# Optimization experiments

Hardware: AMD Instinct MI355X
Metric: run time of the kernel (lower is better)

## Reference

```python
import jax, jax.numpy as jnp
import numpy as np

C = 96        # d_model
DI = 192      # d_inner = 2*C
N = 16        # d_state
R = 6         # dt_rank = ceil(C/16)
K = 4         # scan directions
B_, H_, W_ = 2, 48, 48


def setup_inputs():
    key = jax.random.key(0)
    ks = jax.random.split(key, 12)
    def rn(k, shape, s=0.02):
        return jax.random.normal(k, shape, jnp.float32) * s
    # S4D-real A init and realistic dt bias (inverse softplus of dt in [1e-3, 1e-1])
    A = jnp.tile(jnp.arange(1, N + 1, dtype=jnp.float32), (K, DI, 1))
    dt = jax.random.uniform(ks[0], (K, DI), jnp.float32, 1e-3, 1e-1)
    inv_softplus_dt = dt + jnp.log(-jnp.expm1(-dt))
    return {
        "x": jax.random.normal(ks[1], (B_, C, H_, W_), jnp.float32),
        "ln1_w": jnp.ones((C,), jnp.float32), "ln1_b": jnp.zeros((C,), jnp.float32),
        "in_proj_w": rn(ks[2], (2 * DI, C)),
        "conv_w": rn(ks[3], (DI, 1, 3, 3), 0.1), "conv_b": jnp.zeros((DI,), jnp.float32),
        "x_proj_w": rn(ks[4], (K, R + 2 * N, DI)),
        "dt_proj_w": rn(ks[5], (K, DI, R), 0.1), "dt_proj_b": inv_softplus_dt,
        "A_log": jnp.log(A), "Ds": jnp.ones((K, DI), jnp.float32),
        "out_norm_w": jnp.ones((DI,), jnp.float32), "out_norm_b": jnp.zeros((DI,), jnp.float32),
        "out_proj_w": rn(ks[6], (C, DI)),
        "ln2_w": jnp.ones((C,), jnp.float32), "ln2_b": jnp.zeros((C,), jnp.float32),
        "fc1_w": rn(ks[7], (C, C)), "fc1_b": jnp.zeros((C,), jnp.float32),
        "fc2_w": rn(ks[8], (C, C)), "fc2_b": jnp.zeros((C,), jnp.float32),
        "proj_w": rn(ks[9], (1, C)), "proj_b": jnp.zeros((1,), jnp.float32),
    }


def _layernorm(x, w, b, eps=1e-5):
    mu = x.mean(-1, keepdims=True)
    var = x.var(-1, keepdims=True)
    return (x - mu) * jax.lax.rsqrt(var + eps) * w + b


def _selective_scan(u, delta, A, Bm, Cm, D):
    # u, delta: (B,K,D,L); A: (K,D,N); Bm, Cm: (B,K,N,L); D: (K,D)
    dA = jnp.exp(jnp.einsum('bkdl,kdn->lbkdn', delta, A))
    dBu = jnp.einsum('bkdl,bknl->lbkdn', delta * u, Bm)
    Ct = jnp.moveaxis(Cm, -1, 0)  # (L,B,K,N)
    h0 = jnp.zeros(dA.shape[1:], u.dtype)
    def step(h, inp):
        dA_t, dBu_t, C_t = inp
        h = dA_t * h + dBu_t
        y = jnp.einsum('bkdn,bkn->bkd', h, C_t)
        return h, y
    _, ys = jax.lax.scan(step, h0, (dA, dBu, Ct))
    y = jnp.moveaxis(ys, 0, -1)  # (B,K,D,L)
    return y + u * D[None, :, :, None]


def _ss2d(x, in_proj_w, conv_w, conv_b, x_proj_w, dt_proj_w, dt_proj_b,
          A_log, Ds, out_norm_w, out_norm_b, out_proj_w):
    Bsz, H, W, _ = x.shape
    L = H * W
    xz = x @ in_proj_w.T                      # (B,H,W,2*DI)
    xh, z = jnp.split(xz, 2, axis=-1)
    xc = xh.transpose(0, 3, 1, 2)             # (B,DI,H,W)
    xc = jax.lax.conv_general_dilated(
        xc, conv_w, (1, 1), ((1, 1), (1, 1)),
        feature_group_count=DI,
        dimension_numbers=('NCHW', 'OIHW', 'NCHW')) + conv_b[None, :, None, None]
    xc = jax.nn.silu(xc)
    # cross-scan: 4 directions (row-major, col-major, and their reverses)
    xf = xc.reshape(Bsz, DI, L)
    xt = xc.transpose(0, 1, 3, 2).reshape(Bsz, DI, L)
    xs2 = jnp.stack([xf, xt], axis=1)
    xs = jnp.concatenate([xs2, jnp.flip(xs2, axis=-1)], axis=1)   # (B,4,DI,L)
    x_dbl = jnp.einsum('bkdl,kcd->bkcl', xs, x_proj_w)
    dts, Bm, Cm = jnp.split(x_dbl, [R, R + N], axis=2)
    delta = jnp.einsum('bkrl,kdr->bkdl', dts, dt_proj_w) + dt_proj_b[None, :, :, None]
    delta = jax.nn.softplus(delta)
    A = -jnp.exp(A_log)
    out_y = _selective_scan(xs, delta, A, Bm, Cm, Ds)             # (B,4,DI,L)
    # cross-merge: undo flips/transposes and sum
    inv_y = jnp.flip(out_y[:, 2:4], axis=-1)
    wh_y = out_y[:, 1].reshape(Bsz, DI, W, H).transpose(0, 1, 3, 2).reshape(Bsz, DI, L)
    invwh_y = inv_y[:, 1].reshape(Bsz, DI, W, H).transpose(0, 1, 3, 2).reshape(Bsz, DI, L)
    y = out_y[:, 0] + inv_y[:, 0] + wh_y + invwh_y                # (B,DI,L)
    y = _layernorm(y.transpose(0, 2, 1), out_norm_w, out_norm_b).reshape(Bsz, H, W, DI)
    y = y * jax.nn.silu(z)
    return y @ out_proj_w.T


def reference(x, ln1_w, ln1_b, in_proj_w, conv_w, conv_b, x_proj_w, dt_proj_w,
              dt_proj_b, A_log, Ds, out_norm_w, out_norm_b, out_proj_w,
              ln2_w, ln2_b, fc1_w, fc1_b, fc2_w, fc2_b, proj_w, proj_b):
    xh = x.transpose(0, 2, 3, 1)   # (B,H,W,C)
    # VSSBlock (pre-norm): x = x + SS2D(LN(x)); x = x + MLP(LN(x))
    h1 = _layernorm(xh, ln1_w, ln1_b)
    xh = xh + _ss2d(h1, in_proj_w, conv_w, conv_b, x_proj_w, dt_proj_w,
                    dt_proj_b, A_log, Ds, out_norm_w, out_norm_b, out_proj_w)
    h2 = _layernorm(xh, ln2_w, ln2_b)
    xh = xh + (jax.nn.gelu(h2 @ fc1_w.T + fc1_b, approximate=False) @ fc2_w.T + fc2_b)
    # 1x1 conv projector + sigmoid
    y = xh @ proj_w.T + proj_b     # (B,H,W,1)
    return jax.nn.sigmoid(y).transpose(0, 3, 1, 2)
```

## Files before the change

kernel.cpp:

```cpp
#include <hip/hip_runtime.h>
#include <cstdint>

static constexpr int LSZ = 2304;
static constexpr int CBS = 96;
static constexpr int DIN = 192;
static constexpr int NST = 16;
static constexpr int HHT = 48;
static constexpr int WWD = 48;
static constexpr int CHN = 16;
static constexpr int CHL = 144;

static constexpr size_t OFF_XCONV = 0;
static constexpr size_t OFF_SILUZ = 884736;
static constexpr size_t OFF_XC    = 1769472;
static constexpr size_t OFF_XCT   = 2654208;
static constexpr size_t OFF_BCT   = 3686400;
static constexpr size_t OFF_DELTA = 4276224;
static constexpr size_t OFF_YK    = 7815168;
static constexpr size_t OFF_WT    = 11796480;

__device__ __forceinline__ float f4get(const float4& v, int i) {
    return i == 0 ? v.x : i == 1 ? v.y : i == 2 ? v.z : v.w;
}

__device__ __forceinline__ float rotadd16(float v) {
    int m;
    m = __builtin_amdgcn_update_dpp(0, __float_as_int(v), 0x128, 0xf, 0xf, false); v += __int_as_float(m);
    m = __builtin_amdgcn_update_dpp(0, __float_as_int(v), 0x124, 0xf, 0xf, false); v += __int_as_float(m);
    m = __builtin_amdgcn_update_dpp(0, __float_as_int(v), 0x122, 0xf, 0xf, false); v += __int_as_float(m);
    m = __builtin_amdgcn_update_dpp(0, __float_as_int(v), 0x121, 0xf, 0xf, false); v += __int_as_float(m);
    return v;
}

__global__ __launch_bounds__(256) void kPrep(const float* __restrict__ Wp,
    const float* __restrict__ Wo, const float* __restrict__ W1,
    const float* __restrict__ W2, float* __restrict__ wt) {
    int e = blockIdx.x * 256 + threadIdx.x;
    if (e < 36864) {
        int c = e / 384, t = e % 384;
        wt[e] = Wp[t * 96 + c];
    } else if (e < 55296) {
        int e2 = e - 36864; int dd = e2 / 96, cc = e2 % 96;
        wt[e] = Wo[cc * 192 + dd];
    } else if (e < 64512) {
        int e2 = e - 55296; int jj = e2 / 96, ii = e2 % 96;
        wt[e] = W1[ii * 96 + jj];
    } else if (e < 73728) {
        int e2 = e - 64512; int jj = e2 / 96, ii = e2 % 96;
        wt[e] = W2[ii * 96 + jj];
    }
}

__global__ __launch_bounds__(384) void kA(const float* __restrict__ x,
    const float* __restrict__ ln1w, const float* __restrict__ ln1b,
    const float* __restrict__ Wt, float* __restrict__ xconv, float* __restrict__ siluz) {
    int blk = blockIdx.x; int b = blk / 144; int s0 = (blk % 144) * 16;
    int tid = threadIdx.x;
    __shared__ float xln[96][20];
    __shared__ float mu16[16], ir16[16];
#pragma unroll
    for (int it = 0; it < 4; ++it) {
        int e = it * 384 + tid; int c = e >> 4, si = e & 15;
        xln[c][si] = x[((size_t)b * CBS + c) * LSZ + s0 + si];
    }
    __syncthreads();
    if (tid < 16) {
        float s1 = 0.f, s2 = 0.f;
#pragma unroll 8
        for (int c = 0; c < 96; ++c) { float v = xln[c][tid]; s1 += v; s2 += v * v; }
        float mu = s1 * (1.f / 96.f);
        mu16[tid] = mu; ir16[tid] = rsqrtf(s2 * (1.f / 96.f) - mu * mu + 1e-5f);
    }
    __syncthreads();
#pragma unroll
    for (int it = 0; it < 4; ++it) {
        int e = it * 384 + tid; int c = e >> 4, si = e & 15;
        xln[c][si] = (xln[c][si] - mu16[si]) * ir16[si] * ln1w[c] + ln1b[c];
    }
    __syncthreads();
    float acc[16];
#pragma unroll
    for (int i = 0; i < 16; ++i) acc[i] = 0.f;
    for (int c = 0; c < 96; ++c) {
        float wv = Wt[c * 384 + tid];
#pragma unroll
        for (int i = 0; i < 16; ++i) acc[i] = fmaf(wv, xln[c][i], acc[i]);
    }
    if (tid < DIN) {
        size_t base = ((size_t)b * DIN + tid) * LSZ + s0;
#pragma unroll
        for (int q = 0; q < 4; ++q) {
            float4 v = make_float4(acc[4 * q], acc[4 * q + 1], acc[4 * q + 2], acc[4 * q + 3]);
            *(float4*)(xconv + base + 4 * q) = v;
        }
    } else {
        int t = tid - DIN;
#pragma unroll
        for (int si = 0; si < 16; ++si) {
            float z = acc[si];
            siluz[((size_t)b * LSZ + s0 + si) * DIN + t] = z / (1.f + __expf(-z));
        }
    }
}

__global__ __launch_bounds__(256) void kB(const float* __restrict__ xconv,
    const float* __restrict__ cw, const float* __restrict__ cb,
    float* __restrict__ xc, float* __restrict__ xcT) {
    int bd = blockIdx.x;
    int d = bd % DIN;
    int tid = threadIdx.x;
    __shared__ float inp[2304];
    __shared__ float outp[48 * 49];
    const float* src = xconv + (size_t)bd * LSZ;
#pragma unroll
    for (int i = 0; i < 9; ++i) inp[i * 256 + tid] = src[i * 256 + tid];
    float w0 = cw[d * 9 + 0], w1 = cw[d * 9 + 1], w2 = cw[d * 9 + 2];
    float w3 = cw[d * 9 + 3], w4 = cw[d * 9 + 4], w5 = cw[d * 9 + 5];
    float w6 = cw[d * 9 + 6], w7 = cw[d * 9 + 7], w8 = cw[d * 9 + 8];
    float bias = cb[d];
    __syncthreads();
#pragma unroll
    for (int i = 0; i < 9; ++i) {
        int s = i * 256 + tid; int h = s / 48, w = s % 48;
        float acc = bias;
        bool hn = h > 0, hp = h < 47, wn = w > 0, wp = w < 47;
        if (hn) {
            if (wn) acc = fmaf(inp[s - 49], w0, acc);
            acc = fmaf(inp[s - 48], w1, acc);
            if (wp) acc = fmaf(inp[s - 47], w2, acc);
        }
        if (wn) acc = fmaf(inp[s - 1], w3, acc);
        acc = fmaf(inp[s], w4, acc);
        if (wp) acc = fmaf(inp[s + 1], w5, acc);
        if (hp) {
            if (wn) acc = fmaf(inp[s + 47], w6, acc);
            acc = fmaf(inp[s + 48], w7, acc);
            if (wp) acc = fmaf(inp[s + 49], w8, acc);
        }
        float r = acc / (1.f + __expf(-acc));
        xc[(size_t)bd * LSZ + s] = r;
        outp[h * 49 + w] = r;
    }
    __syncthreads();
#pragma unroll
    for (int i = 0; i < 9; ++i) {
        int p = i * 256 + tid;
        int w = p / 48, h = p % 48;
        xcT[(size_t)bd * LSZ + p] = outp[h * 49 + w];
    }
}

__global__ __launch_bounds__(256) void kC(const float* __restrict__ xc,
    const float* __restrict__ xcT, const float* __restrict__ xpw,
    const float* __restrict__ dtw, const float* __restrict__ dtb,
    float* __restrict__ BCt, float* __restrict__ delta) {
    int blk = blockIdx.x; int lt = blk % 36; int k = (blk / 36) & 3; int b = blk / 144;
    int l0 = lt * 64;
    int bk = b * 4 + k;
    __shared__ float xs[DIN][64];
    __shared__ float stage[64][33];
    __shared__ float dtrL[6][64];
    __shared__ float wsh[DIN * 6];
    __shared__ float bshL[DIN];
    const float* src = ((k & 1) ? xcT : xc) + (size_t)b * DIN * LSZ;
    bool fwd = (k < 2);
    int tid = threadIdx.x;
    for (int e = tid; e < 1152; e += 256) wsh[e] = dtw[k * 1152 + e];
    if (tid < DIN) bshL[tid] = dtb[k * DIN + tid];
#pragma unroll
    for (int i = 0; i < 48; ++i) {
        int e = i * 256 + tid; int d = e >> 6, ll = e & 63;
        int l = l0 + ll; int sl = fwd ? l : (LSZ - 1 - l);
        xs[d][ll] = src[(size_t)d * LSZ + sl];
    }
    __syncthreads();
    int c0 = tid >> 6, ll = tid & 63;
    float acc[10];
#pragma unroll
    for (int j = 0; j < 10; ++j) acc[j] = 0.f;
    for (int d0 = 0; d0 < DIN; d0 += 16) {
        float xv[16];
#pragma unroll
        for (int i = 0; i < 16; ++i) xv[i] = xs[d0 + i][ll];
#pragma unroll
        for (int j = 0; j < 10; ++j) {
            int c = j * 4 + c0;
            if (c < 38) {
                const float4* wr = (const float4*)(xpw + ((size_t)(k * 38 + c)) * DIN + d0);
                float4 q0 = wr[0], q1 = wr[1], q2 = wr[2], q3 = wr[3];
                acc[j] += xv[0] * q0.x + xv[1] * q0.y + xv[2] * q0.z + xv[3] * q0.w
                        + xv[4] * q1.x + xv[5] * q1.y + xv[6] * q1.z + xv[7] * q1.w
                        + xv[8] * q2.x + xv[9] * q2.y + xv[10] * q2.z + xv[11] * q2.w
                        + xv[12] * q3.x + xv[13] * q3.y + xv[14] * q3.z + xv[15] * q3.w;
            }
        }
    }
#pragma unroll
    for (int j = 0; j < 10; ++j) {
        int c = j * 4 + c0;
        if (c < 6) {
            dtrL[c][ll] = acc[j];
        } else if (c < 38) {
            int n2 = (c < 22) ? (c - 6) : (16 + c - 22);
            stage[ll][n2] = acc[j];
        }
    }
    __syncthreads();
    float* dst = BCt + ((size_t)bk * LSZ + l0) * 32;
#pragma unroll
    for (int it = 0; it < 8; ++it) {
        int e = it * 256 + tid;
        int l = e >> 5, n2 = e & 31;
        dst[e] = stage[l][n2];
    }
    int dsub = tid >> 6;
    float dr[6];
#pragma unroll
    for (int r = 0; r < 6; ++r) dr[r] = dtrL[r][ll];
    for (int j = 0; j < 48; ++j) {
        int d = j * 4 + dsub;
        float a2 = bshL[d];
#pragma unroll
        for (int r = 0; r < 6; ++r) a2 = fmaf(dr[r], wsh[d * 6 + r], a2);
        float sp = (a2 > 20.f) ? a2 : log1pf(__expf(a2));
        delta[((size_t)bk * DIN + d) * LSZ + l0 + ll] = sp;
    }
}

__global__ __launch_bounds__(256, 4) void kD(const float* __restrict__ delta,
    const float* __restrict__ xc, const float* __restrict__ xcT,
    const float* __restrict__ BCt, const float* __restrict__ A_log, float* __restrict__ yk) {
    int g = blockIdx.x;
    int tid = threadIdx.x;
    int n = tid & 15; int c = tid >> 4;
    int d = g % DIN; int bk = g / DIN; int k = bk & 3; int b = bk >> 2;
    __shared__ float hfinL[256];
    __shared__ float sumdL[16];
    __shared__ float hinL[256];

    float An2 = -__expf(A_log[((size_t)(k * DIN + d)) * NST + n]) * 1.44269504f;
    const float* ub = ((k & 1) ? xcT : xc) + ((size_t)(b * DIN + d)) * LSZ;
    bool fwd = (k < 2);
    int l0 = c * CHL;
    const float* dp = delta + (size_t)g * LSZ + l0;
    const float* up = fwd ? (ub + l0) : (ub + (LSZ - 4) - l0);
    const float* bc = BCt + ((size_t)bk * LSZ + l0) * 32 + n;

    float h = 0.f, sd = 0.f;
    for (int j0 = 0; j0 < CHL; j0 += 4) {
        float4 dv = *(const float4*)(dp + j0);
        float4 uv;
        if (fwd) uv = *(const float4*)(up + j0);
        else { float4 tv = *(const float4*)(up - j0); uv = make_float4(tv.w, tv.z, tv.y, tv.x); }
#pragma unroll
        for (int jj = 0; jj < 4; ++jj) {
            float bn = bc[(j0 + jj) * 32];
            float dl = f4get(dv, jj);
            float da = __builtin_amdgcn_exp2f(dl * An2);
            h = fmaf(da, h, dl * f4get(uv, jj) * bn);
            sd += dl;
        }
    }
    hfinL[tid] = h;
    if (n == 0) sumdL[c] = sd;
    __syncthreads();

    if (tid < 16) {
        float hh = 0.f;
#pragma unroll
        for (int cc = 0; cc < 16; ++cc) {
            hinL[cc * 16 + tid] = hh;
            hh = fmaf(__builtin_amdgcn_exp2f(An2 * sumdL[cc]), hh, hfinL[cc * 16 + tid]);
        }
    }
    __syncthreads();

    h = hinL[tid];
    float* yo = yk + (size_t)g * LSZ + l0 + n;
    for (int m = 0; m < 9; ++m) {
        float ykeep = 0.f;
        for (int q = 0; q < 4; ++q) {
            int j0 = m * 16 + q * 4;
            float4 dv = *(const float4*)(dp + j0);
            float4 uv;
            if (fwd) uv = *(const float4*)(up + j0);
            else { float4 tv = *(const float4*)(up - j0); uv = make_float4(tv.w, tv.z, tv.y, tv.x); }
#pragma unroll
            for (int jj = 0; jj < 4; ++jj) {
                float bn = bc[(j0 + jj) * 32];
                float cn = bc[(j0 + jj) * 32 + 16];
                float dl = f4get(dv, jj);
                float da = __builtin_amdgcn_exp2f(dl * An2);
                h = fmaf(da, h, dl * f4get(uv, jj) * bn);
                float p = rotadd16(h * cn);
                ykeep = (n == q * 4 + jj) ? p : ykeep;
            }
        }
        yo[m * 16] = ykeep;
    }
}

__global__ __launch_bounds__(256) void kM(const float* __restrict__ yk,
    const float* __restrict__ xc, const float* __restrict__ Dsp, float* __restrict__ ym) {
    int blk = blockIdx.x;
    int b = blk / DIN; int d = blk % DIN;
    int tid = threadIdx.x;
    __shared__ float buf[4][48 * 49];
    float Dsum = Dsp[d] + Dsp[DIN + d] + Dsp[2 * DIN + d] + Dsp[3 * DIN + d];
#pragma unroll
    for (int kk = 0; kk < 4; ++kk) {
        const float* src = yk + ((size_t)((b * 4 + kk) * DIN + d)) * LSZ;
#pragma unroll
        for (int i = 0; i < 9; ++i) {
            int s = i * 256 + tid;
            buf[kk][s + s / 48] = src[s];
        }
    }
    __syncthreads();
    const float* xrow = xc + ((size_t)(b * DIN + d)) * LSZ;
    float* dst = ym + ((size_t)blk) * LSZ;
#pragma unroll
    for (int i = 0; i < 9; ++i) {
        int s = i * 256 + tid; int hh = s / 48, ww = s % 48;
        float v0 = buf[0][hh * 49 + ww];
        float v2 = buf[2][(47 - hh) * 49 + (47 - ww)];
        float v1 = buf[1][ww * 49 + hh];
        float v3 = buf[3][(47 - ww) * 49 + (47 - hh)];
        dst[s] = v0 + v2 + v1 + v3 + Dsum * xrow[s];
    }
}

__global__ __launch_bounds__(192) void kEF(const float* __restrict__ ym,
    const float* __restrict__ siluz, const float* __restrict__ x,
    const float* __restrict__ onw, const float* __restrict__ onb,
    const float* __restrict__ WoT,
    const float* __restrict__ l2w, const float* __restrict__ l2b,
    const float* __restrict__ W1T, const float* __restrict__ b1,
    const float* __restrict__ W2T, const float* __restrict__ b2,
    const float* __restrict__ pw, const float* __restrict__ pb, float* __restrict__ out) {
    int blk = blockIdx.x; int b = blk / 144; int s0 = (blk % 144) * 16;
    int tid = threadIdx.x;
    __shared__ float yl[DIN][17];
    __shared__ float xo[96][17];
    __shared__ float aa[96][17];
    __shared__ float mu16[16], ir16[16];
#pragma unroll
    for (int it = 0; it < 16; ++it) {
        int e = it * 192 + tid; int d = e >> 4, si = e & 15;
        yl[d][si] = ym[((size_t)(b * DIN + d)) * LSZ + s0 + si];
    }
    __syncthreads();
    if (tid < 16) {
        float s1 = 0.f, s2 = 0.f;
        for (int c = 0; c < DIN; ++c) { float v = yl[c][tid]; s1 += v; s2 += v * v; }
        float mu = s1 * (1.f / 192.f);
        mu16[tid] = mu; ir16[tid] = rsqrtf(s2 * (1.f / 192.f) - mu * mu + 1e-5f);
    }
    __syncthreads();
#pragma unroll
    for (int si = 0; si < 16; ++si) {
        float v = yl[tid][si];
        v = (v - mu16[si]) * ir16[si] * onw[tid] + onb[tid];
        yl[tid][si] = v * siluz[((size_t)b * LSZ + s0 + si) * DIN + tid];
    }
    __syncthreads();
    int tp = tid % 96, half = tid / 96;
    {
        float acc[8];
#pragma unroll
        for (int i = 0; i < 8; ++i) acc[i] = 0.f;
        for (int d2 = 0; d2 < DIN; ++d2) {
            float wv = WoT[d2 * 96 + tp];
#pragma unroll
            for (int i = 0; i < 8; ++i) acc[i] = fmaf(wv, yl[d2][half * 8 + i], acc[i]);
        }
#pragma unroll
        for (int i = 0; i < 8; ++i) {
            int si = half * 8 + i;
            xo[tp][si] = x[((size_t)b * CBS + tp) * LSZ + s0 + si] + acc[i];
        }
    }
    __syncthreads();
    if (tid < 16) {
        float s1 = 0.f, s2 = 0.f;
        for (int c = 0; c < 96; ++c) { float v = xo[c][tid]; s1 += v; s2 += v * v; }
        float mu = s1 * (1.f / 96.f);
        mu16[tid] = mu; ir16[tid] = rsqrtf(s2 * (1.f / 96.f) - mu * mu + 1e-5f);
    }
    __syncthreads();
#pragma unroll
    for (int it = 0; it < 8; ++it) {
        int e = it * 192 + tid; int si = e / 96, cc = e % 96;
        aa[cc][si] = (xo[cc][si] - mu16[si]) * ir16[si] * l2w[cc] + l2b[cc];
    }
    __syncthreads();
    float acc[8];
#pragma unroll
    for (int i = 0; i < 8; ++i) acc[i] = 0.f;
    for (int j = 0; j < 96; ++j) {
        float wv = W1T[j * 96 + tp];
#pragma unroll
        for (int i = 0; i < 8; ++i) acc[i] = fmaf(wv, aa[j][half * 8 + i], acc[i]);
    }
    __syncthreads();
#pragma unroll
    for (int i = 0; i < 8; ++i) {
        float tv = acc[i] + b1[tp];
        aa[tp][half * 8 + i] = 0.5f * tv * (1.f + erff(tv * 0.70710678118654752f));
    }
    __syncthreads();
    float acc2[8];
#pragma unroll
    for (int i = 0; i < 8; ++i) acc2[i] = 0.f;
    for (int j = 0; j < 96; ++j) {
        float wv = W2T[j * 96 + tp];
#pragma unroll
        for (int i = 0; i < 8; ++i) acc2[i] = fmaf(wv, aa[j][half * 8 + i], acc2[i]);
    }
    __syncthreads();
#pragma unroll
    for (int i = 0; i < 8; ++i) {
        float xf = xo[tp][half * 8 + i] + acc2[i] + b2[tp];
        aa[tp][half * 8 + i] = xf * pw[tp];
    }
    __syncthreads();
    if (tid < 16) {
        float ssum = 0.f;
        for (int c = 0; c < 96; ++c) ssum += aa[c][tid];
        out[(size_t)b * LSZ + s0 + tid] = 1.f / (1.f + __expf(-(ssum + pb[0])));
    }
}

extern "C" void kernel_launch(void* const* d_in, const int* in_sizes, int n_in,
                              void* d_out, int out_size, void* d_ws, size_t ws_size,
                              hipStream_t stream) {
    const float* x    = (const float*)d_in[0];
    const float* ln1w = (const float*)d_in[1];
    const float* ln1b = (const float*)d_in[2];
    const float* Wp   = (const float*)d_in[3];
    const float* cw   = (const float*)d_in[4];
    const float* cb   = (const float*)d_in[5];
    const float* xpw  = (const float*)d_in[6];
    const float* dtw  = (const float*)d_in[7];
    const float* dtb  = (const float*)d_in[8];
    const float* Alog = (const float*)d_in[9];
    const float* Dsp  = (const float*)d_in[10];
    const float* onw  = (const float*)d_in[11];
    const float* onb  = (const float*)d_in[12];
    const float* Wo   = (const float*)d_in[13];
    const float* l2w  = (const float*)d_in[14];
    const float* l2b  = (const float*)d_in[15];
    const float* W1   = (const float*)d_in[16];
    const float* b1   = (const float*)d_in[17];
    const float* W2   = (const float*)d_in[18];
    const float* b2   = (const float*)d_in[19];
    const float* pw   = (const float*)d_in[20];
    const float* pb   = (const float*)d_in[21];

    float* ws    = (float*)d_ws;
    float* xconv = ws + OFF_XCONV;
    float* ym    = ws + OFF_XCONV;
    float* siluz = ws + OFF_SILUZ;
    float* xc    = ws + OFF_XC;
    float* xcT   = ws + OFF_XCT;
    float* BCt   = ws + OFF_BCT;
    float* delta = ws + OFF_DELTA;
    float* yk    = ws + OFF_YK;
    float* wt    = ws + OFF_WT;
    float* WoT   = wt + 36864;
    float* W1T   = wt + 55296;
    float* W2T   = wt + 64512;

    kPrep<<<288, 256, 0, stream>>>(Wp, Wo, W1, W2, wt);
    kA<<<288, 384, 0, stream>>>(x, ln1w, ln1b, wt, xconv, siluz);
    kB<<<384, 256, 0, stream>>>(xconv, cw, cb, xc, xcT);
    kC<<<288, 256, 0, stream>>>(xc, xcT, xpw, dtw, dtb, BCt, delta);
    kD<<<1536, 256, 0, stream>>>(delta, xc, xcT, BCt, Alog, yk);
    kM<<<384, 256, 0, stream>>>(yk, xc, Dsp, ym);
    kEF<<<288, 192, 0, stream>>>(ym, siluz, x, onw, onb, WoT,
                                 l2w, l2b, W1T, b1, W2T, b2, pw, pb, (float*)d_out);
}
```

Measured before the change: 180.3 us.

## Split-K the in_proj and output/MLP matmuls and interleave B/C in scan layout

kA now runs 768 threads and splits the 96-wide reduction into two halves, combining the partial sums through shared memory. kEF likewise doubles its threads to 384 and splits each of its three matmuls (out_proj, fc1, fc2) over two K-halves with a shared reduction buffer. Separately, the B and C values in the BCt buffer are interleaved per state, so the scan kernel fetches both with one float2 load. This aims to raise occupancy and latency hiding in kernels that only launch 288 blocks, at the cost of extra shared memory, more barriers and reduction traffic.

```diff
diff --git a/kernel.cpp b/kernel.cpp
--- a/kernel.cpp
+++ b/kernel.cpp
@@ -51,16 +51,17 @@
     }
 }
 
-__global__ __launch_bounds__(384) void kA(const float* __restrict__ x,
+__global__ __launch_bounds__(768) void kA(const float* __restrict__ x,
     const float* __restrict__ ln1w, const float* __restrict__ ln1b,
     const float* __restrict__ Wt, float* __restrict__ xconv, float* __restrict__ siluz) {
     int blk = blockIdx.x; int b = blk / 144; int s0 = (blk % 144) * 16;
     int tid = threadIdx.x;
     __shared__ float xln[96][20];
+    __shared__ float redA[384][17];
     __shared__ float mu16[16], ir16[16];
 #pragma unroll
-    for (int it = 0; it < 4; ++it) {
-        int e = it * 384 + tid; int c = e >> 4, si = e & 15;
+    for (int it = 0; it < 2; ++it) {
+        int e = it * 768 + tid; int c = e >> 4, si = e & 15;
         xln[c][si] = x[((size_t)b * CBS + c) * LSZ + s0 + si];
     }
     __syncthreads();
@@ -73,32 +74,42 @@
     }
     __syncthreads();
 #pragma unroll
-    for (int it = 0; it < 4; ++it) {
-        int e = it * 384 + tid; int c = e >> 4, si = e & 15;
+    for (int it = 0; it < 2; ++it) {
+        int e = it * 768 + tid; int c = e >> 4, si = e & 15;
         xln[c][si] = (xln[c][si] - mu16[si]) * ir16[si] * ln1w[c] + ln1b[c];
     }
     __syncthreads();
+    int t = tid % 384, cg = tid / 384;
     float acc[16];
 #pragma unroll
     for (int i = 0; i < 16; ++i) acc[i] = 0.f;
-    for (int c = 0; c < 96; ++c) {
-        float wv = Wt[c * 384 + tid];
+    for (int c = cg * 48; c < cg * 48 + 48; ++c) {
+        float wv = Wt[c * 384 + t];
 #pragma unroll
         for (int i = 0; i < 16; ++i) acc[i] = fmaf(wv, xln[c][i], acc[i]);
     }
-    if (tid < DIN) {
-        size_t base = ((size_t)b * DIN + tid) * LSZ + s0;
-#pragma unroll
-        for (int q = 0; q < 4; ++q) {
-            float4 v = make_float4(acc[4 * q], acc[4 * q + 1], acc[4 * q + 2], acc[4 * q + 3]);
-            *(float4*)(xconv + base + 4 * q) = v;
-        }
-    } else {
-        int t = tid - DIN;
-#pragma unroll
-        for (int si = 0; si < 16; ++si) {
-            float z = acc[si];
-            siluz[((size_t)b * LSZ + s0 + si) * DIN + t] = z / (1.f + __expf(-z));
+    if (cg == 1) {
+#pragma unroll
+        for (int i = 0; i < 16; ++i) redA[t][i] = acc[i];
+    }
+    __syncthreads();
+    if (cg == 0) {
+#pragma unroll
+        for (int i = 0; i < 16; ++i) acc[i] += redA[t][i];
+        if (t < DIN) {
+            size_t base = ((size_t)b * DIN + t) * LSZ + s0;
+#pragma unroll
+            for (int q = 0; q < 4; ++q) {
+                float4 v = make_float4(acc[4 * q], acc[4 * q + 1], acc[4 * q + 2], acc[4 * q + 3]);
+                *(float4*)(xconv + base + 4 * q) = v;
+            }
+        } else {
+            int tz = t - DIN;
+#pragma unroll
+            for (int si = 0; si < 16; ++si) {
+                float z = acc[si];
+                siluz[((size_t)b * LSZ + s0 + si) * DIN + tz] = z / (1.f + __expf(-z));
+            }
         }
     }
 }
@@ -201,7 +212,7 @@
         if (c < 6) {
             dtrL[c][ll] = acc[j];
         } else if (c < 38) {
-            int n2 = (c < 22) ? (c - 6) : (16 + c - 22);
+            int n2 = (c < 22) ? (2 * (c - 6)) : (2 * (c - 22) + 1);
             stage[ll][n2] = acc[j];
         }
     }
@@ -244,7 +255,7 @@
     int l0 = c * CHL;
     const float* dp = delta + (size_t)g * LSZ + l0;
     const float* up = fwd ? (ub + l0) : (ub + (LSZ - 4) - l0);
-    const float* bc = BCt + ((size_t)bk * LSZ + l0) * 32 + n;
+    const float* bc = BCt + ((size_t)bk * LSZ + l0) * 32 + n * 2;
 
     float h = 0.f, sd = 0.f;
     for (int j0 = 0; j0 < CHL; j0 += 4) {
@@ -254,10 +265,10 @@
         else { float4 tv = *(const float4*)(up - j0); uv = make_float4(tv.w, tv.z, tv.y, tv.x); }
 #pragma unroll
         for (int jj = 0; jj < 4; ++jj) {
-            float bn = bc[(j0 + jj) * 32];
+            float2 bcv = *(const float2*)(bc + (j0 + jj) * 32);
             float dl = f4get(dv, jj);
             float da = __builtin_amdgcn_exp2f(dl * An2);
-            h = fmaf(da, h, dl * f4get(uv, jj) * bn);
+            h = fmaf(da, h, dl * f4get(uv, jj) * bcv.x);
             sd += dl;
         }
     }
@@ -287,12 +298,11 @@
             else { float4 tv = *(const float4*)(up - j0); uv = make_float4(tv.w, tv.z, tv.y, tv.x); }
 #pragma unroll
             for (int jj = 0; jj < 4; ++jj) {
-                float bn = bc[(j0 + jj) * 32];
-                float cn = bc[(j0 + jj) * 32 + 16];
+                float2 bcv = *(const float2*)(bc + (j0 + jj) * 32);
                 float dl = f4get(dv, jj);
                 float da = __builtin_amdgcn_exp2f(dl * An2);
-                h = fmaf(da, h, dl * f4get(uv, jj) * bn);
-                float p = rotadd16(h * cn);
+                h = fmaf(da, h, dl * f4get(uv, jj) * bcv.x);
+                float p = rotadd16(h * bcv.y);
                 ykeep = (n == q * 4 + jj) ? p : ykeep;
             }
         }
@@ -330,7 +340,7 @@
     }
 }
 
-__global__ __launch_bounds__(192) void kEF(const float* __restrict__ ym,
+__global__ __launch_bounds__(384) void kEF(const float* __restrict__ ym,
     const float* __restrict__ siluz, const float* __restrict__ x,
     const float* __restrict__ onw, const float* __restrict__ onb,
     const float* __restrict__ WoT,
@@ -343,10 +353,11 @@
     __shared__ float yl[DIN][17];
     __shared__ float xo[96][17];
     __shared__ float aa[96][17];
+    __shared__ float red[384][9];
     __shared__ float mu16[16], ir16[16];
 #pragma unroll
-    for (int it = 0; it < 16; ++it) {
-        int e = it * 192 + tid; int d = e >> 4, si = e & 15;
+    for (int it = 0; it < 8; ++it) {
+        int e = it * 384 + tid; int d = e >> 4, si = e & 15;
         yl[d][si] = ym[((size_t)(b * DIN + d)) * LSZ + s0 + si];
     }
     __syncthreads();
@@ -357,27 +368,36 @@
         mu16[tid] = mu; ir16[tid] = rsqrtf(s2 * (1.f / 192.f) - mu * mu + 1e-5f);
     }
     __syncthreads();
-#pragma unroll
-    for (int si = 0; si < 16; ++si) {
-        float v = yl[tid][si];
-        v = (v - mu16[si]) * ir16[si] * onw[tid] + onb[tid];
-        yl[tid][si] = v * siluz[((size_t)b * LSZ + s0 + si) * DIN + tid];
-    }
-    __syncthreads();
-    int tp = tid % 96, half = tid / 96;
+    {
+        int d = tid % 192, sh = tid / 192;
+#pragma unroll
+        for (int i = 0; i < 8; ++i) {
+            int si = sh * 8 + i;
+            float v = yl[d][si];
+            v = (v - mu16[si]) * ir16[si] * onw[d] + onb[d];
+            yl[d][si] = v * siluz[((size_t)b * LSZ + s0 + si) * DIN + d];
+        }
+    }
+    __syncthreads();
+    int tp = tid % 96, half = (tid / 96) & 1, kg = tid / 192;
     {
         float acc[8];
 #pragma unroll
         for (int i = 0; i < 8; ++i) acc[i] = 0.f;
-        for (int d2 = 0; d2 < DIN; ++d2) {
+        for (int d2 = kg * 96; d2 < kg * 96 + 96; ++d2) {
             float wv = WoT[d2 * 96 + tp];
 #pragma unroll
             for (int i = 0; i < 8; ++i) acc[i] = fmaf(wv, yl[d2][half * 8 + i], acc[i]);
         }
+#pragma unroll
+        for (int i = 0; i < 8; ++i) red[tid][i] = acc[i];
+    }
+    __syncthreads();
+    if (tid < 192) {
 #pragma unroll
         for (int i = 0; i < 8; ++i) {
             int si = half * 8 + i;
-            xo[tp][si] = x[((size_t)b * CBS + tp) * LSZ + s0 + si] + acc[i];
+            xo[tp][si] = x[((size_t)b * CBS + tp) * LSZ + s0 + si] + red[tid][i] + red[tid + 192][i];
         }
     }
     __syncthreads();
@@ -389,39 +409,51 @@
     }
     __syncthreads();
 #pragma unroll
-    for (int it = 0; it < 8; ++it) {
-        int e = it * 192 + tid; int si = e / 96, cc = e % 96;
+    for (int it = 0; it < 4; ++it) {
+        int e = it * 384 + tid; int si = e / 96, cc = e % 96;
         aa[cc][si] = (xo[cc][si] - mu16[si]) * ir16[si] * l2w[cc] + l2b[cc];
     }
     __syncthreads();
-    float acc[8];
-#pragma unroll
-    for (int i = 0; i < 8; ++i) acc[i] = 0.f;
-    for (int j = 0; j < 96; ++j) {
-        float wv = W1T[j * 96 + tp];
-#pragma unroll
-        for (int i = 0; i < 8; ++i) acc[i] = fmaf(wv, aa[j][half * 8 + i], acc[i]);
-    }
-    __syncthreads();
-#pragma unroll
-    for (int i = 0; i < 8; ++i) {
-        float tv = acc[i] + b1[tp];
-        aa[tp][half * 8 + i] = 0.5f * tv * (1.f + erff(tv * 0.70710678118654752f));
-    }
-    __syncthreads();
-    float acc2[8];
-#pragma unroll
-    for (int i = 0; i < 8; ++i) acc2[i] = 0.f;
-    for (int j = 0; j < 96; ++j) {
-        float wv = W2T[j * 96 + tp];
-#pragma unroll
-        for (int i = 0; i < 8; ++i) acc2[i] = fmaf(wv, aa[j][half * 8 + i], acc2[i]);
-    }
-    __syncthreads();
-#pragma unroll
-    for (int i = 0; i < 8; ++i) {
-        float xf = xo[tp][half * 8 + i] + acc2[i] + b2[tp];
-        aa[tp][half * 8 + i] = xf * pw[tp];
+    {
+        float acc[8];
+#pragma unroll
+        for (int i = 0; i < 8; ++i) acc[i] = 0.f;
+        for (int j = kg * 48; j < kg * 48 + 48; ++j) {
+            float wv = W1T[j * 96 + tp];
+#pragma unroll
+            for (int i = 0; i < 8; ++i) acc[i] = fmaf(wv, aa[j][half * 8 + i], acc[i]);
+        }
+#pragma unroll
+        for (int i = 0; i < 8; ++i) red[tid][i] = acc[i];
+    }
+    __syncthreads();
+    if (tid < 192) {
+#pragma unroll
+        for (int i = 0; i < 8; ++i) {
+            float tv = red[tid][i] + red[tid + 192][i] + b1[tp];
+            aa[tp][half * 8 + i] = 0.5f * tv * (1.f + erff(tv * 0.70710678118654752f));
+        }
+    }
+    __syncthreads();
+    {
+        float acc2[8];
+#pragma unroll
+        for (int i = 0; i < 8; ++i) acc2[i] = 0.f;
+        for (int j = kg * 48; j < kg * 48 + 48; ++j) {
+            float wv = W2T[j * 96 + tp];
+#pragma unroll
+            for (int i = 0; i < 8; ++i) acc2[i] = fmaf(wv, aa[j][half * 8 + i], acc2[i]);
+        }
+#pragma unroll
+        for (int i = 0; i < 8; ++i) red[tid][i] = acc2[i];
+    }
+    __syncthreads();
+    if (tid < 192) {
+#pragma unroll
+        for (int i = 0; i < 8; ++i) {
+            float xf = xo[tp][half * 8 + i] + red[tid][i] + red[tid + 192][i] + b2[tp];
+            aa[tp][half * 8 + i] = xf * pw[tp];
+        }
     }
     __syncthreads();
     if (tid < 16) {
@@ -472,11 +504,11 @@
     float* W2T   = wt + 64512;
 
     kPrep<<<288, 256, 0, stream>>>(Wp, Wo, W1, W2, wt);
-    kA<<<288, 384, 0, stream>>>(x, ln1w, ln1b, wt, xconv, siluz);
+    kA<<<288, 768, 0, stream>>>(x, ln1w, ln1b, wt, xconv, siluz);
     kB<<<384, 256, 0, stream>>>(xconv, cw, cb, xc, xcT);
     kC<<<288, 256, 0, stream>>>(xc, xcT, xpw, dtw, dtb, BCt, delta);
     kD<<<1536, 256, 0, stream>>>(delta, xc, xcT, BCt, Alog, yk);
     kM<<<384, 256, 0, stream>>>(yk, xc, Dsp, ym);
-    kEF<<<288, 192, 0, stream>>>(ym, siluz, x, onw, onb, WoT,
+    kEF<<<288, 384, 0, stream>>>(ym, siluz, x, onw, onb, WoT,
                                  l2w, l2b, W1T, b1, W2T, b2, pw, pb, (float*)d_out);
 }
```

Measured after the change: 197.8 us. +9.7%, slower.
